# Kernel optimization log

Hardware: AMD Instinct MI355X
Metric: run time of the kernel (lower is better)

Reference implementation:

```python
import jax, jax.numpy as jnp
import numpy as np

B, C_IN, C_MID, C_OUT, H, W = 256, 2, 128, 64, 15, 15
N_RES = 4  # line_length//2 - 1 with line_length=11

# per-direction input offsets for kernel taps w0 and w2 (w1 is always center),
# matching fix_direction_order=True sparse 3x3 kernel construction:
# dir0 horizontal, dir1 vertical, dir2 anti-diagonal, dir3 main diagonal.
OFFSETS = (((0, -1), (0, 1)),
           ((-1, 0), (1, 0)),
           ((1, -1), (-1, 1)),
           ((-1, -1), (1, 1)))


def shift2d(x, di, dj):
    # out[..., i, j] = x[..., i+di, j+dj] with zero padding (di,dj in {-1,0,1})
    nd = x.ndim
    xp = jnp.pad(x, [(0, 0)] * (nd - 2) + [(1, 1), (1, 1)])
    h, w = x.shape[-2], x.shape[-1]
    return xp[..., 1 + di:1 + di + h, 1 + dj:1 + dj + w]


def dir_conv(x, w, b):
    # x: [4,B,Cin,H,W]; w: [Cout,Cin,3]; b: [Cout]
    x0 = jnp.stack([shift2d(x[d], *OFFSETS[d][0]) for d in range(4)])
    x2 = jnp.stack([shift2d(x[d], *OFFSETS[d][1]) for d in range(4)])
    y = (jnp.einsum('oc,dbchw->dbohw', w[..., 0], x0)
         + jnp.einsum('oc,dbchw->dbohw', w[..., 1], x)
         + jnp.einsum('oc,dbchw->dbohw', w[..., 2], x2))
    return y + b[None, None, :, None, None]


def conv1x1(x, w, b):
    # x: [4,B,Cin,H,W]; w: [Cout,Cin]; b: [Cout]
    return jnp.einsum('oc,dbchw->dbohw', w, x) + b[None, None, :, None, None]


def setup_inputs() -> dict:
    key = jax.random.key(0)
    ks = jax.random.split(key, 16)
    s_in = 1.0 / np.sqrt(3 * C_IN)
    s_mid = 1.0 / np.sqrt(3 * C_MID)
    s_pw = 1.0 / np.sqrt(C_MID)
    return {
        'x': jax.random.normal(ks[0], (B, C_IN, H, W), jnp.float32),
        'dconv0_w': jax.random.normal(ks[1], (C_MID, C_IN, 3), jnp.float32) * s_in,
        'dconv0_b': jnp.zeros((C_MID,), jnp.float32),
        'res_dconv_w': jax.random.normal(ks[2], (N_RES, C_MID, C_MID, 3), jnp.float32) * s_mid,
        'res_dconv_b': jnp.zeros((N_RES, C_MID), jnp.float32),
        'res_pw_w': jax.random.normal(ks[3], (N_RES, C_MID, C_MID), jnp.float32) * s_pw,
        'res_pw_b': jnp.zeros((N_RES, C_MID), jnp.float32),
        'c0_w1': jax.random.normal(ks[4], (C_MID, C_MID), jnp.float32) * s_pw,
        'c0_b1': jnp.zeros((C_MID,), jnp.float32),
        'c0_w2': jax.random.normal(ks[5], (C_MID, C_MID), jnp.float32) * s_pw,
        'c0_b2': jnp.zeros((C_MID,), jnp.float32),
        'final_w': jax.random.normal(ks[6], (C_OUT, C_MID), jnp.float32) * s_pw,
        'final_b': jnp.zeros((C_OUT,), jnp.float32),
    }


def reference(x, dconv0_w, dconv0_b, res_dconv_w, res_dconv_b,
              res_pw_w, res_pw_b, c0_w1, c0_b1, c0_w2, c0_b2,
              final_w, final_b):
    act = jax.nn.silu
    # all 4 direction streams start from the same input plane
    h = jnp.broadcast_to(x[None], (4,) + x.shape)  # [4,B,Cin,H,W]
    h = act(dir_conv(h, dconv0_w, dconv0_b))
    # DirectionalConvResBlocks (norm='none')
    for i in range(N_RES):
        r = h
        h = act(dir_conv(h, res_dconv_w[i], res_dconv_b[i]))
        h = act(conv1x1(h, res_pw_w[i], res_pw_b[i]))
        h = h + r
    # Conv0dResBlock (two 1x1 convs, middle_dim_multipler=1)
    r = h
    h = act(conv1x1(h, c0_w1, c0_b1))
    h = act(conv1x1(h, c0_w2, c0_b2))
    h = h + r
    # final 1x1 conv, then stack directions at dim=1 -> [B,4,Cout,H,W]
    h = conv1x1(h, final_w, final_b)
    return jnp.transpose(h, (1, 0, 2, 3, 4))
```

## Files before the change

kernel.cpp:

```cpp
#include <hip/hip_runtime.h>

using u16 = unsigned short;
using u32 = unsigned int;

typedef __bf16 bf16x8 __attribute__((ext_vector_type(8)));
typedef float  f32x4  __attribute__((ext_vector_type(4)));

#define NPOS   225
#define NT     15
#define ROWP   136
#define A_ROWS 289
#define B_ROWS 241
#define A_ELEMS (A_ROWS*ROWP)
#define B_ELEMS (B_ROWS*ROWP)
#define LDS_BYTES ((A_ELEMS + B_ELEMS)*2)
#define RSTRIDE17 (17*ROWP)

#define WA_PER_L 49152
#define WP_OFF   (4*WA_PER_L)
#define WP_PER   16384
#define WF_OFF   (WP_OFF + 6*WP_PER)
#define W_U16_TOTAL (WF_OFF + 8192)

__host__ __device__ __forceinline__ int permc(int c){
  return (c & ~0x3C) | (((c >> 2) & 3) << 4) | (((c >> 4) & 3) << 2);
}

__device__ __forceinline__ float bflo(u32 q){ return __uint_as_float(q << 16); }
__device__ __forceinline__ float bfhi(u32 q){ return __uint_as_float(q & 0xffff0000u); }
__device__ __forceinline__ u16 f2bf(float f){
  u32 u = __float_as_uint(f);
  return (u16)((u + 0x7fffu + ((u >> 16) & 1u)) >> 16);
}
__device__ __forceinline__ u32 packbf(float a, float b){
  union { __bf16 h[2]; u32 u; } r;
  r.h[0] = (__bf16)a; r.h[1] = (__bf16)b;
  return r.u;
}
__device__ __forceinline__ float silu_f(float x){
  return x * __builtin_amdgcn_rcpf(1.f + __expf(-x));
}
__device__ __forceinline__ f32x4 mfma16(bf16x8 a, bf16x8 b, f32x4 c){
  return __builtin_amdgcn_mfma_f32_16x16x32_bf16(a, b, c, 0, 0, 0);
}

__global__ void prep_w(const float* __restrict__ d0w, const float* __restrict__ d0b,
                       const float* __restrict__ rdw,
                       const float* __restrict__ rpw, const float* __restrict__ c1w,
                       const float* __restrict__ c2w, const float* __restrict__ fw,
                       float* __restrict__ ws)
{
  u16* wsb = (u16*)(ws + 896);
  const int total = 896 + W_U16_TOTAL;
  for (int idx = blockIdx.x*blockDim.x + threadIdx.x; idx < total; idx += gridDim.x*blockDim.x){
    if (idx < 768){
      int k = idx >> 7, s = idx & 127;
      ws[idx] = d0w[permc(s)*6 + k];
      continue;
    }
    if (idx < 896){
      int s = idx - 768;
      ws[idx] = d0b[permc(s)];
      continue;
    }
    int e = idx - 896;
    float v;
    if (e < WP_OFF){
      int L = e / WA_PER_L, r = e % WA_PER_L;
      int og = r / 24576; int r1 = r - og*24576;
      int tap = r1 >> 13; int r2 = r1 & 8191;
      int ot = r2 >> 11, kb = (r2 >> 9) & 3, l = (r2 >> 3) & 63, j = r2 & 7;
      int o = (og*4 + ot)*16 + (l & 15);
      int ks = kb*32 + ((l >> 4) << 3) + j;
      v = rdw[((L*128 + o)*128 + permc(ks))*3 + tap];
    } else if (e < WF_OFF){
      int t2 = e - WP_OFF;
      int i = t2 / WP_PER, r = t2 % WP_PER;
      int og2 = r >> 13;
      int ot = (r >> 11) & 3, kb = (r >> 9) & 3, l = (r >> 3) & 63, j = r & 7;
      int o = (og2*4 + ot)*16 + (l & 15);
      int ks = kb*32 + ((l >> 4) << 3) + j;
      v = (i < 4) ? rpw[(i*128 + o)*128 + permc(ks)]
        : (i == 4) ? c1w[o*128 + permc(ks)] : c2w[o*128 + permc(ks)];
    } else {
      int e2 = e - WF_OFF;
      int ot = e2 >> 11, kb = (e2 >> 9) & 3, l = (e2 >> 3) & 63, j = e2 & 7;
      int o = ot*16 + (l & 15);
      int ks = kb*32 + ((l >> 4) << 3) + j;
      v = fw[o*128 + permc(ks)];
    }
    wsb[e] = f2bf(v);
  }
}

__device__ __forceinline__ uint4 pack_silu2(const f32x4& a, const f32x4& b){
  uint4 q;
  q.x = packbf(silu_f(a[0]), silu_f(a[1]));
  q.y = packbf(silu_f(a[2]), silu_f(a[3]));
  q.z = packbf(silu_f(b[0]), silu_f(b[1]));
  q.w = packbf(silu_f(b[2]), silu_f(b[3]));
  return q;
}

template<int NTL>
__device__ __forceinline__ void dconv_mfma(const u16* __restrict__ As, u16* __restrict__ Bs,
    const u16* __restrict__ wloc, const float* __restrict__ bias,
    int lane, int og, int T0, int off0, int off2)
{
  const int col = lane & 15, kg = lane >> 4, koff = kg*8;
  f32x4 acc[4][NTL];
  #pragma unroll
  for (int ot=0; ot<4; ++ot){
    f32x4 bz = *(const f32x4*)(bias + og*64 + ot*16 + kg*4);
    #pragma unroll
    for (int t=0;t<NTL;++t) acc[ot][t] = bz;
  }
  const int c1 = (col+1)*ROWP + koff;
  #pragma unroll 1
  for (int tap=0; tap<3; ++tap){
    const int offr = (tap==0) ? off0 : (tap==1) ? 0 : off2;
    bf16x8 w[4][4];
    #pragma unroll
    for (int ot=0; ot<4; ++ot)
      #pragma unroll
      for (int kb=0; kb<4; ++kb)
        w[ot][kb] = *(const bf16x8*)(wloc + tap*8192 + ot*2048 + kb*512 + lane*8);
    #pragma unroll
    for (int t=0; t<NTL; ++t){
      const u16* s = As + (T0+t+1)*RSTRIDE17 + c1 + offr;
      __builtin_amdgcn_s_setprio(1);
      #pragma unroll
      for (int kb=0; kb<4; ++kb){
        bf16x8 v = *(const bf16x8*)(s + kb*32);
        acc[0][t] = mfma16(w[0][kb], v, acc[0][t]);
        acc[1][t] = mfma16(w[1][kb], v, acc[1][t]);
        acc[2][t] = mfma16(w[2][kb], v, acc[2][t]);
        acc[3][t] = mfma16(w[3][kb], v, acc[3][t]);
      }
      __builtin_amdgcn_s_setprio(0);
    }
  }
  if (col < 15){
    #pragma unroll
    for (int t=0;t<NTL;++t){
      u16* dp = Bs + ((T0+t)*16+col)*ROWP + og*64 + kg*16;
      uint4 q0 = pack_silu2(acc[0][t], acc[1][t]);
      uint4 q1 = pack_silu2(acc[2][t], acc[3][t]);
      *(uint4*)dp = q0;
      *(uint4*)(dp+8) = q1;
    }
  }
}

template<bool SRC_HALO, bool DST_HALO, bool RESID>
__device__ __forceinline__ void pw_mfma(const u16* __restrict__ src, u16* __restrict__ dst,
    const u16* __restrict__ wloc, const float* __restrict__ bias,
    int lane, int og2, int T0, int T1)
{
  const int col = lane & 15, kg = lane >> 4, koff = kg*8;
  bf16x8 wp[4][4];
  #pragma unroll
  for (int ot=0; ot<4; ++ot)
    #pragma unroll
    for (int kb=0; kb<4; ++kb)
      wp[ot][kb] = *(const bf16x8*)(wloc + og2*8192 + ot*2048 + kb*512 + lane*8);
  f32x4 bz[4];
  #pragma unroll
  for (int ot=0; ot<4; ++ot) bz[ot] = *(const f32x4*)(bias + og2*64 + ot*16 + kg*4);
  const int c1 = (col+1)*ROWP;
  #pragma unroll 2
  for (int tile=T0; tile<T1; ++tile){
    const int rh = (tile+1)*RSTRIDE17 + c1;
    const int rc = (tile*16+col)*ROWP;
    const u16* S = src + (SRC_HALO ? rh : rc) + koff;
    f32x4 a0 = bz[0], a1 = bz[1], a2 = bz[2], a3 = bz[3];
    __builtin_amdgcn_s_setprio(1);
    #pragma unroll
    for (int kb=0; kb<4; ++kb){
      bf16x8 v = *(const bf16x8*)(S + kb*32);
      a0 = mfma16(wp[0][kb], v, a0);
      a1 = mfma16(wp[1][kb], v, a1);
      a2 = mfma16(wp[2][kb], v, a2);
      a3 = mfma16(wp[3][kb], v, a3);
    }
    __builtin_amdgcn_s_setprio(0);
    if (col < 15){
      u16* dp = dst + (DST_HALO ? rh : rc) + og2*64 + kg*16;
      float s0 = silu_f(a0[0]), s1 = silu_f(a0[1]), s2 = silu_f(a0[2]), s3 = silu_f(a0[3]);
      float s4 = silu_f(a1[0]), s5 = silu_f(a1[1]), s6 = silu_f(a1[2]), s7 = silu_f(a1[3]);
      float s8 = silu_f(a2[0]), s9 = silu_f(a2[1]), sa = silu_f(a2[2]), sb = silu_f(a2[3]);
      float sc = silu_f(a3[0]), sd = silu_f(a3[1]), se = silu_f(a3[2]), sf = silu_f(a3[3]);
      if (RESID){
        uint4 r0 = *(const uint4*)dp;
        uint4 r1 = *(const uint4*)(dp+8);
        s0 += bflo(r0.x); s1 += bfhi(r0.x); s2 += bflo(r0.y); s3 += bfhi(r0.y);
        s4 += bflo(r0.z); s5 += bfhi(r0.z); s6 += bflo(r0.w); s7 += bfhi(r0.w);
        s8 += bflo(r1.x); s9 += bfhi(r1.x); sa += bflo(r1.y); sb += bfhi(r1.y);
        sc += bflo(r1.z); sd += bfhi(r1.z); se += bflo(r1.w); sf += bfhi(r1.w);
      }
      uint4 q0, q1;
      q0.x = packbf(s0, s1); q0.y = packbf(s2, s3);
      q0.z = packbf(s4, s5); q0.w = packbf(s6, s7);
      q1.x = packbf(s8, s9); q1.y = packbf(sa, sb);
      q1.z = packbf(sc, sd); q1.w = packbf(se, sf);
      *(uint4*)dp = q0;
      *(uint4*)(dp+8) = q1;
    }
  }
}

__device__ __forceinline__ void fin_mfma(const u16* __restrict__ As,
    const u16* __restrict__ wloc, const float* __restrict__ bias,
    float* __restrict__ out, int lane, int ogf, int T0, int T1, int bd)
{
  const int col = lane & 15, kg = lane >> 4, koff = kg*8;
  bf16x8 wf[2][4];
  #pragma unroll
  for (int ot=0; ot<2; ++ot)
    #pragma unroll
    for (int kb=0; kb<4; ++kb)
      wf[ot][kb] = *(const bf16x8*)(wloc + (ogf*2+ot)*2048 + kb*512 + lane*8);
  f32x4 bz0 = *(const f32x4*)(bias + ogf*32 + kg*4);
  f32x4 bz1 = *(const f32x4*)(bias + ogf*32 + 16 + kg*4);
  const int c1 = (col+1)*ROWP;
  #pragma unroll 1
  for (int tile=T0; tile<T1; ++tile){
    const u16* S = As + (tile+1)*RSTRIDE17 + c1 + koff;
    f32x4 a0 = bz0, a1 = bz1;
    __builtin_amdgcn_s_setprio(1);
    #pragma unroll
    for (int kb=0; kb<4; ++kb){
      bf16x8 v = *(const bf16x8*)(S + kb*32);
      a0 = mfma16(wf[0][kb], v, a0);
      a1 = mfma16(wf[1][kb], v, a1);
    }
    __builtin_amdgcn_s_setprio(0);
    if (col < 15){
      float* op = out + ((size_t)(bd*64 + ogf*32 + kg*4))*NPOS + tile*15 + col;
      op[0]      = a0[0];
      op[NPOS]   = a0[1];
      op[2*NPOS] = a0[2];
      op[3*NPOS] = a0[3];
      float* oq = op + 16*NPOS;
      oq[0]      = a1[0];
      oq[NPOS]   = a1[1];
      oq[2*NPOS] = a1[2];
      oq[3*NPOS] = a1[3];
    }
  }
}

__global__ void __launch_bounds__(768, 3)
mix9_main(const float* __restrict__ x,
          const float* __restrict__ b_rd,
          const float* __restrict__ b_rp,
          const float* __restrict__ b_c1,
          const float* __restrict__ b_c2,
          const float* __restrict__ b_fin,
          const float* __restrict__ wt,
          float* __restrict__ out)
{
  extern __shared__ u16 sm[];
  u16* As = sm;
  u16* Bs = sm + A_ELEMS;

  const int blk  = blockIdx.x;
  const int b    = blk >> 2, d = blk & 3;
  const int tid  = threadIdx.x;
  const int wave = __builtin_amdgcn_readfirstlane(tid >> 6);
  const int lane = tid & 63;

  const int og   = (wave >= 6) ? 1 : 0;
  const int pg   = wave - og*6;
  const int T0p  = (pg < 3) ? pg*3 : 9 + (pg-3)*2;
  const int T1p  = T0p + ((pg < 3) ? 3 : 2);

  const int DI0[4] = {0,-1, 1,-1}, DJ0[4] = {-1, 0,-1,-1};
  const int DI2[4] = {0, 1,-1, 1}, DJ2[4] = { 1, 0, 1, 1};
  const int di0 = DI0[d], dj0 = DJ0[d], di2 = DI2[d], dj2 = DJ2[d];
  const int off0 = (di0*17 + dj0)*ROWP;
  const int off2 = (di2*17 + dj2)*ROWP;

  for (int k2 = tid; k2 < A_ELEMS; k2 += 768) As[k2] = 0;
  float* xs = (float*)Bs;
  for (int k2 = tid; k2 < 2*NPOS; k2 += 768) xs[k2] = x[b*(2*NPOS) + k2];
  __syncthreads();

  if (wave < 8){
    const float* b0p = wt + 768;
    const int ob = wave * 16;
    #pragma unroll 1
    for (int pb = 0; pb < 4; ++pb){
      int pp = pb*64 + lane;
      int i = pp >> 4, j = pp & 15;
      if (i >= 15 || j >= 15) continue;
      float acc[16];
      #pragma unroll
      for (int oo=0;oo<16;++oo) acc[oo] = b0p[ob+oo];
      #pragma unroll
      for (int c=0;c<2;++c){
        int i0=i+di0, j0=j+dj0, i2=i+di2, j2=j+dj2;
        float x0 = ((unsigned)i0<15u && (unsigned)j0<15u) ? xs[c*NPOS + i0*15 + j0] : 0.f;
        float x1 = xs[c*NPOS + i*15 + j];
        float x2 = ((unsigned)i2<15u && (unsigned)j2<15u) ? xs[c*NPOS + i2*15 + j2] : 0.f;
        const float* w0r = wt + (c*3+0)*128 + ob;
        const float* w1r = wt + (c*3+1)*128 + ob;
        const float* w2r = wt + (c*3+2)*128 + ob;
        #pragma unroll
        for (int oo=0;oo<16;++oo)
          acc[oo] = fmaf(w0r[oo],x0, fmaf(w1r[oo],x1, fmaf(w2r[oo],x2, acc[oo])));
      }
      u16* dp = As + ((i+1)*17 + (j+1))*ROWP + ob;
      #pragma unroll
      for (int oo=0;oo<16;oo+=2)
        *(u32*)(dp+oo) = packbf(silu_f(acc[oo]), silu_f(acc[oo+1]));
    }
  }
  __syncthreads();

  const u16* wsb = (const u16*)(wt + 896);

  #pragma unroll 1
  for (int L = 0; L < 4; ++L){
    if (pg < 3)
      dconv_mfma<3>(As, Bs, wsb + L*WA_PER_L + og*24576, b_rd + L*128, lane, og, pg*3, off0, off2);
    else
      dconv_mfma<2>(As, Bs, wsb + L*WA_PER_L + og*24576, b_rd + L*128, lane, og, 9 + (pg-3)*2, off0, off2);
    __syncthreads();
    pw_mfma<false,true,true>(Bs, As, wsb + WP_OFF + L*WP_PER, b_rp + L*128, lane, og, T0p, T1p);
    __syncthreads();
  }

  pw_mfma<true,false,false>(As, Bs, wsb + WP_OFF + 4*WP_PER, b_c1, lane, og, T0p, T1p);
  __syncthreads();
  pw_mfma<false,true,true>(Bs, As, wsb + WP_OFF + 5*WP_PER, b_c2, lane, og, T0p, T1p);
  __syncthreads();

  fin_mfma(As, wsb + WF_OFF, b_fin, out, lane, og, T0p, T1p, b*4 + d);
}

extern "C" void kernel_launch(void* const* d_in, const int* in_sizes, int n_in,
                              void* d_out, int out_size, void* d_ws, size_t ws_size,
                              hipStream_t stream)
{
  const float* x     = (const float*)d_in[0];
  const float* w_d0  = (const float*)d_in[1];
  const float* b_d0  = (const float*)d_in[2];
  const float* w_rd  = (const float*)d_in[3];
  const float* b_rd  = (const float*)d_in[4];
  const float* w_rp  = (const float*)d_in[5];
  const float* b_rp  = (const float*)d_in[6];
  const float* w_c1  = (const float*)d_in[7];
  const float* b_c1  = (const float*)d_in[8];
  const float* w_c2  = (const float*)d_in[9];
  const float* b_c2  = (const float*)d_in[10];
  const float* w_fin = (const float*)d_in[11];
  const float* b_fin = (const float*)d_in[12];
  float* wt  = (float*)d_ws;
  float* out = (float*)d_out;

  prep_w<<<128, 512, 0, stream>>>(w_d0, b_d0, w_rd, w_rp, w_c1, w_c2, w_fin, wt);

  (void)hipFuncSetAttribute((const void*)mix9_main,
                            hipFuncAttributeMaxDynamicSharedMemorySize, LDS_BYTES);
  mix9_main<<<1024, 768, LDS_BYTES, stream>>>(x, b_rd, b_rp, b_c1, b_c2, b_fin, wt, out);
}
```

Measured before the change: 239.8 us.

## Prefetch next stage's first weight fragments into registers across barriers

Each stage now loads the first half of the next stage's weight fragments from global memory into registers (ping-pong preA/preB) before the barrier. The following stage consumes these preloaded registers, so part of the weight-load latency overlaps with the current stage's compute and the sync. The first dconv layer's weights are prefetched during LDS init, and the final conv's weights come entirely from the prefetch. This raises register pressure by 16 bf16x8 vectors per lane, which could hurt occupancy or cause spills.

```diff
diff --git a/kernel.cpp b/kernel.cpp
--- a/kernel.cpp
+++ b/kernel.cpp
@@ -42,6 +42,14 @@
 }
 __device__ __forceinline__ f32x4 mfma16(bf16x8 a, bf16x8 b, f32x4 c){
   return __builtin_amdgcn_mfma_f32_16x16x32_bf16(a, b, c, 0, 0, 0);
+}
+
+__device__ __forceinline__ void pre8(bf16x8 (&p)[2][4], const u16* base, int lane){
+  #pragma unroll
+  for (int o=0;o<2;++o)
+    #pragma unroll
+    for (int k=0;k<4;++k)
+      p[o][k] = *(const bf16x8*)(base + o*2048 + k*512 + lane*8);
 }
 
 __global__ void prep_w(const float* __restrict__ d0w, const float* __restrict__ d0b,
@@ -105,7 +113,8 @@
 template<int NTL>
 __device__ __forceinline__ void dconv_mfma(const u16* __restrict__ As, u16* __restrict__ Bs,
     const u16* __restrict__ wloc, const float* __restrict__ bias,
-    int lane, int og, int T0, int off0, int off2)
+    int lane, int og, int T0, int off0, int off2,
+    const bf16x8 (&pre0)[2][4], const u16* __restrict__ nx, bf16x8 (&preN)[2][4])
 {
   const int col = lane & 15, kg = lane >> 4, koff = kg*8;
   f32x4 acc[4][NTL];
@@ -120,11 +129,21 @@
   for (int tap=0; tap<3; ++tap){
     const int offr = (tap==0) ? off0 : (tap==1) ? 0 : off2;
     bf16x8 w[4][4];
-    #pragma unroll
-    for (int ot=0; ot<4; ++ot)
-      #pragma unroll
-      for (int kb=0; kb<4; ++kb)
-        w[ot][kb] = *(const bf16x8*)(wloc + tap*8192 + ot*2048 + kb*512 + lane*8);
+    if (tap == 0){
+      #pragma unroll
+      for (int kb=0; kb<4; ++kb){ w[0][kb] = pre0[0][kb]; w[1][kb] = pre0[1][kb]; }
+      #pragma unroll
+      for (int ot=2; ot<4; ++ot)
+        #pragma unroll
+        for (int kb=0; kb<4; ++kb)
+          w[ot][kb] = *(const bf16x8*)(wloc + ot*2048 + kb*512 + lane*8);
+    } else {
+      #pragma unroll
+      for (int ot=0; ot<4; ++ot)
+        #pragma unroll
+        for (int kb=0; kb<4; ++kb)
+          w[ot][kb] = *(const bf16x8*)(wloc + tap*8192 + ot*2048 + kb*512 + lane*8);
+    }
     #pragma unroll
     for (int t=0; t<NTL; ++t){
       const u16* s = As + (T0+t+1)*RSTRIDE17 + c1 + offr;
@@ -140,6 +159,7 @@
       __builtin_amdgcn_s_setprio(0);
     }
   }
+  pre8(preN, nx, lane);
   if (col < 15){
     #pragma unroll
     for (int t=0;t<NTL;++t){
@@ -155,15 +175,19 @@
 template<bool SRC_HALO, bool DST_HALO, bool RESID>
 __device__ __forceinline__ void pw_mfma(const u16* __restrict__ src, u16* __restrict__ dst,
     const u16* __restrict__ wloc, const float* __restrict__ bias,
-    int lane, int og2, int T0, int T1)
+    int lane, int og2, int T0, int T1,
+    const bf16x8 (&pre0)[2][4], const u16* __restrict__ nx, bf16x8 (&preN)[2][4])
 {
   const int col = lane & 15, kg = lane >> 4, koff = kg*8;
+  pre8(preN, nx, lane);
   bf16x8 wp[4][4];
   #pragma unroll
-  for (int ot=0; ot<4; ++ot)
+  for (int kb=0; kb<4; ++kb){ wp[0][kb] = pre0[0][kb]; wp[1][kb] = pre0[1][kb]; }
+  #pragma unroll
+  for (int ot=2; ot<4; ++ot)
     #pragma unroll
     for (int kb=0; kb<4; ++kb)
-      wp[ot][kb] = *(const bf16x8*)(wloc + og2*8192 + ot*2048 + kb*512 + lane*8);
+      wp[ot][kb] = *(const bf16x8*)(wloc + ot*2048 + kb*512 + lane*8);
   f32x4 bz[4];
   #pragma unroll
   for (int ot=0; ot<4; ++ot) bz[ot] = *(const f32x4*)(bias + og2*64 + ot*16 + kg*4);
@@ -210,16 +234,10 @@
 }
 
 __device__ __forceinline__ void fin_mfma(const u16* __restrict__ As,
-    const u16* __restrict__ wloc, const float* __restrict__ bias,
-    float* __restrict__ out, int lane, int ogf, int T0, int T1, int bd)
+    const float* __restrict__ bias, float* __restrict__ out,
+    int lane, int ogf, int T0, int T1, int bd, const bf16x8 (&wf)[2][4])
 {
   const int col = lane & 15, kg = lane >> 4, koff = kg*8;
-  bf16x8 wf[2][4];
-  #pragma unroll
-  for (int ot=0; ot<2; ++ot)
-    #pragma unroll
-    for (int kb=0; kb<4; ++kb)
-      wf[ot][kb] = *(const bf16x8*)(wloc + (ogf*2+ot)*2048 + kb*512 + lane*8);
   f32x4 bz0 = *(const f32x4*)(bias + ogf*32 + kg*4);
   f32x4 bz1 = *(const f32x4*)(bias + ogf*32 + 16 + kg*4);
   const int c1 = (col+1)*ROWP;
@@ -280,6 +298,10 @@
   const int di0 = DI0[d], dj0 = DJ0[d], di2 = DI2[d], dj2 = DJ2[d];
   const int off0 = (di0*17 + dj0)*ROWP;
   const int off2 = (di2*17 + dj2)*ROWP;
+
+  const u16* wsb = (const u16*)(wt + 896);
+  bf16x8 preA[2][4], preB[2][4];
+  pre8(preA, wsb + og*24576, lane);
 
   for (int k2 = tid; k2 < A_ELEMS; k2 += 768) As[k2] = 0;
   float* xs = (float*)Bs;
@@ -318,25 +340,28 @@
   }
   __syncthreads();
 
-  const u16* wsb = (const u16*)(wt + 896);
-
   #pragma unroll 1
   for (int L = 0; L < 4; ++L){
+    const u16* wd = wsb + L*WA_PER_L + og*24576;
+    const u16* wp = wsb + WP_OFF + L*WP_PER + og*8192;
+    const u16* nx = (L < 3) ? wsb + (L+1)*WA_PER_L + og*24576
+                            : wsb + WP_OFF + 4*WP_PER + og*8192;
     if (pg < 3)
-      dconv_mfma<3>(As, Bs, wsb + L*WA_PER_L + og*24576, b_rd + L*128, lane, og, pg*3, off0, off2);
+      dconv_mfma<3>(As, Bs, wd, b_rd + L*128, lane, og, pg*3, off0, off2, preA, wp, preB);
     else
-      dconv_mfma<2>(As, Bs, wsb + L*WA_PER_L + og*24576, b_rd + L*128, lane, og, 9 + (pg-3)*2, off0, off2);
+      dconv_mfma<2>(As, Bs, wd, b_rd + L*128, lane, og, 9 + (pg-3)*2, off0, off2, preA, wp, preB);
     __syncthreads();
-    pw_mfma<false,true,true>(Bs, As, wsb + WP_OFF + L*WP_PER, b_rp + L*128, lane, og, T0p, T1p);
+    pw_mfma<false,true,true>(Bs, As, wp, b_rp + L*128, lane, og, T0p, T1p, preB, nx, preA);
     __syncthreads();
   }
 
-  pw_mfma<true,false,false>(As, Bs, wsb + WP_OFF + 4*WP_PER, b_c1, lane, og, T0p, T1p);
+  pw_mfma<true,false,false>(As, Bs, wsb + WP_OFF + 4*WP_PER + og*8192, b_c1, lane, og,
+                            T0p, T1p, preA, wsb + WP_OFF + 5*WP_PER + og*8192, preB);
   __syncthreads();
-  pw_mfma<false,true,true>(Bs, As, wsb + WP_OFF + 5*WP_PER, b_c2, lane, og, T0p, T1p);
+  pw_mfma<false,true,true>(Bs, As, wsb + WP_OFF + 5*WP_PER + og*8192, b_c2, lane, og,
+                           T0p, T1p, preB, wsb + WF_OFF + og*4096, preA);
   __syncthreads();
-
-  fin_mfma(As, wsb + WF_OFF, b_fin, out, lane, og, T0p, T1p, b*4 + d);
+  fin_mfma(As, b_fin, out, lane, og, T0p, T1p, b*4 + d, preA);
 }
 
 extern "C" void kernel_launch(void* const* d_in, const int* in_sizes, int n_in,
```

Result: slower. 273.0 us (+13.8%).
